# Kernel tuning notes

Hardware: AMD Instinct MI355X
Metric: run time of the kernel (lower is better)

## Reference

```python
import jax, jax.numpy as jnp
import numpy as np

MAX_AREA_WIDTH = 3  # from init_kwargs


def _window_vals(val, width, merge):
    """Multi-scale forward window sums: for each w in 1..width, sum val[t:t+w]
    over the seq axis, concatenated along the seq axis (total length
    width*L - width*(width-1)/2). Equivalent to the torch recurrence."""
    B, H, L, D = val.shape
    csum = jnp.concatenate(
        [jnp.zeros((B, H, 1, D), val.dtype), jnp.cumsum(val, axis=2)], axis=2)
    parts = []
    for i in range(width):
        w = i + 1
        s = csum[:, :, w:, :] - csum[:, :, :L - w + 1, :]  # [B,H,L-i,D]
        if merge == 'mean':
            s = s / jnp.asarray(w, val.dtype)
        parts.append(s)
    return jnp.concatenate(parts, axis=2)


def _window_masks(mask, width, zero_pad):
    parts = [mask[:, :, :, i:] for i in range(width)]
    m = jnp.concatenate(parts, axis=-1)  # [B,H,L,L']
    if zero_pad:
        m = m.at[:, :, 0, :].set(0)
    return m


def setup_inputs() -> dict:
    key = jax.random.key(0)
    kq, kk, kv = jax.random.split(key, 3)
    B, H, L, D = 8, 8, 512, 64
    q = jax.random.normal(kq, (B, H, L, D), jnp.float32)
    k = jax.random.normal(kk, (B, H, L, D), jnp.float32)
    v = jax.random.normal(kv, (B, H, L, D), jnp.float32)
    # causal attention mask, as used in pykt knowledge-tracing models
    mask = jnp.broadcast_to(jnp.tril(jnp.ones((L, L), jnp.int32)), (B, H, L, L))
    return {"q": q, "k": k, "v": v, "d_k": 64, "mask": mask, "zero_pad": 1}


def reference(q, k, v, d_k, mask, zero_pad):
    W = MAX_AREA_WIDTH
    k_area = _window_vals(k, W, 'mean')   # [B,H,L',D]
    v_area = _window_vals(v, W, 'sum')    # [B,H,L',D]
    m = _window_masks(mask, W, zero_pad)  # [B,H,L,L']
    scores = jnp.einsum('bhqd,bhkd->bhqk', q, k_area) / jnp.sqrt(
        jnp.asarray(d_k, jnp.float32))
    scores = jnp.where(m == 0, jnp.asarray(-1e32, scores.dtype), scores)
    attn = jax.nn.softmax(scores, axis=-1)  # dropout omitted (eval / p=0)
    return jnp.einsum('bhqk,bhkd->bhqd', attn, v_area)
```

## Files before the change

kernel.cpp:

```cpp
#include <hip/hip_runtime.h>


#define LSEQ 512
#define DDIM 64
#define SPB 88
#define SSW 68

typedef __attribute__((ext_vector_type(8))) short bf8_t;
typedef __attribute__((ext_vector_type(4))) float f32x4;

__device__ __forceinline__ unsigned short f2bf(float f) {
  union { float f; unsigned u; } v; v.f = f;
  unsigned u = v.u;
  unsigned r = u + 0x7fffu + ((u >> 16) & 1u);
  return (unsigned short)(r >> 16);
}
__device__ __forceinline__ float bf2f(unsigned short h) {
  union { unsigned u; float f; } v; v.u = ((unsigned)h) << 16; return v.f;
}
__device__ __forceinline__ unsigned pk2(float a, float b) {
  return (unsigned)f2bf(a) | ((unsigned)f2bf(b) << 16);
}
__device__ __forceinline__ float ex2(float x) {
  float r; asm("v_exp_f32 %0, %1" : "=v"(r) : "v"(x)); return r;
}

__global__ __launch_bounds__(256)
void prep_kernel(const float* __restrict__ qg, const float* __restrict__ kg,
                 const float* __restrict__ vg,
                 unsigned short* __restrict__ vt,
                 unsigned short* __restrict__ qbf,
                 unsigned short* __restrict__ kbf,
                 float* __restrict__ outg) {
  const int bid = blockIdx.x, tid = threadIdx.x;
  if (bid < 512) {
    const int bh = bid >> 3, oct = bid & 7;
    const float* vb = vg + (size_t)bh * LSEQ * DDIM;
    unsigned short* vo = vt + (size_t)bh * DDIM * LSEQ;
#pragma unroll
    for (int it = 0; it < 4; ++it) {
      int item = tid + it * 256;
      int d = item & 63, tq = item >> 6;
      int t = oct * 64 + tq * 4;
      ushort4 o;
      o.x = f2bf(vb[(t + 0) * DDIM + d]);
      o.y = f2bf(vb[(t + 1) * DDIM + d]);
      o.z = f2bf(vb[(t + 2) * DDIM + d]);
      o.w = f2bf(vb[(t + 3) * DDIM + d]);
      *(ushort4*)&vo[(size_t)d * LSEQ + t] = o;
    }
  } else if (bid < 1536) {
    const bool isq = bid < 1024;
    const float4* src = (const float4*)(isq ? qg : kg);
    ushort4* dst = (ushort4*)(isq ? qbf : kbf);
    const float s = isq ? 0.125f : 1.0f;
    const int blk = bid & 511;
#pragma unroll
    for (int it = 0; it < 4; ++it) {
      int f = blk * 1024 + it * 256 + tid;
      float4 x = src[f];
      ushort4 o;
      o.x = f2bf(x.x * s); o.y = f2bf(x.y * s);
      o.z = f2bf(x.z * s); o.w = f2bf(x.w * s);
      dst[f] = o;
    }
  } else {
    __shared__ float4 red[256];
    const int bh = bid - 1536;
    const float4* vb4 = (const float4*)(vg + (size_t)bh * LSEQ * DDIM);
    const int d4 = tid & 15, rg = tid >> 4;
    float4 acc = make_float4(0.f, 0.f, 0.f, 0.f);
    for (int t = rg; t < LSEQ; t += 16) {
      float c = (t == 0 || t == LSEQ - 1) ? 3.f
              : (t == 1 || t == LSEQ - 2) ? 5.f : 6.f;
      float4 x = vb4[t * 16 + d4];
      acc.x += c * x.x; acc.y += c * x.y; acc.z += c * x.z; acc.w += c * x.w;
    }
    red[rg * 16 + d4] = acc;
    __syncthreads();
    if (rg == 0) {
      float4 sum = make_float4(0.f, 0.f, 0.f, 0.f);
#pragma unroll
      for (int g = 0; g < 16; ++g) {
        float4 x = red[g * 16 + d4];
        sum.x += x.x; sum.y += x.y; sum.z += x.z; sum.w += x.w;
      }
      const float inv = 1.0f / 1533.0f;
      sum.x *= inv; sum.y *= inv; sum.z *= inv; sum.w *= inv;
      ((float4*)(outg + (size_t)bh * LSEQ * DDIM))[d4] = sum;
    }
  }
}

__global__ __launch_bounds__(256, 4)
void area_task_kernel(const unsigned short* __restrict__ qbf,
                      const unsigned short* __restrict__ kbf,
                      const unsigned short* __restrict__ vtg,
                      float* __restrict__ partials) {
  __shared__ __align__(16) float Ss[4][16][SSW];
  __shared__ __align__(16) unsigned short Ps[4][16 * SPB];

  const int w = threadIdx.x >> 6, lane = threadIdx.x & 63;
  const int tau = blockIdx.x * 4 + w;
  const int bh = tau / 144;
  const int idx = tau - bh * 144;
  int g = 0;
  while (2 * (g + 1) * (g + 2) <= idx) ++g;
  const int rem = idx - 2 * g * (g + 1);
  const int dq = rem / (g + 1);
  const int qt = 4 * g + dq;
  const int kt = rem - dq * (g + 1);
  const int q0 = qt * 16, t0 = kt * 64;

  const int lc = lane & 15, lg = lane >> 4;
  const int koff = lg * 8;
  const int pr = lane >> 2, ps = lane & 3;
  const int ec0 = ps * 16;
  const float L2E = 1.44269504088896341f;

  const unsigned short* qb = qbf + (size_t)bh * LSEQ * DDIM;
  const unsigned short* kb = kbf + (size_t)bh * LSEQ * DDIM;
  const unsigned short* vtb = vtg + (size_t)bh * DDIM * LSEQ;

  const bf8_t qa0 = *(const bf8_t*)&qb[(size_t)(q0 + lc) * DDIM + koff];
  const bf8_t qa1 = *(const bf8_t*)&qb[(size_t)(q0 + lc) * DDIM + 32 + koff];

  float val = 0.f;
  if (kt > 0) {
    const int prr = lane >> 2, jj = (lane >> 1) & 1, hh = lane & 1;
    const unsigned short* qrow = qb + (size_t)(q0 + prr) * DDIM + 32 * hh;
    const unsigned short* krow = kb + (size_t)(t0 - 2 + jj) * DDIM + 32 * hh;
#pragma unroll
    for (int b4 = 0; b4 < 4; ++b4) {
      bf8_t qv = *(const bf8_t*)&qrow[b4 * 8];
      bf8_t kv = *(const bf8_t*)&krow[b4 * 8];
#pragma unroll
      for (int e = 0; e < 8; ++e)
        val = fmaf(bf2f((unsigned short)qv[e]), bf2f((unsigned short)kv[e]), val);
    }
    val += __shfl_xor(val, 1);
  }
  const float ctx2 = __shfl(val, lane & ~3);
  const float ctx1 = __shfl(val, (lane & ~3) | 2);

#pragma unroll
  for (int nt = 0; nt < 4; ++nt) {
    const size_t kr = (size_t)(t0 + nt * 16 + lc) * DDIM;
    bf8_t kf0 = *(const bf8_t*)&kb[kr + koff];
    bf8_t kf1 = *(const bf8_t*)&kb[kr + 32 + koff];
    f32x4 acc = (f32x4){0.f, 0.f, 0.f, 0.f};
    acc = __builtin_amdgcn_mfma_f32_16x16x32_bf16(qa0, kf0, acc, 0, 0, 0);
    acc = __builtin_amdgcn_mfma_f32_16x16x32_bf16(qa1, kf1, acc, 0, 0, 0);
#pragma unroll
    for (int r = 0; r < 4; ++r)
      Ss[w][4 * lg + r][nt * 16 + lc] = acc[r];
  }

  float lrow;
  {
    const int vmax = q0 + pr - t0;
    float pm1, pm2;
    if (ps == 0) {
      pm1 = (kt ? ctx1 : -1.0e30f) * L2E;
      pm2 = (kt ? ctx2 : -1.0e30f) * L2E;
    } else {
      pm1 = Ss[w][pr][ec0 - 1] * L2E;
      pm2 = Ss[w][pr][ec0 - 2] * L2E;
    }

    float sv[16];
    *(float4*)&sv[0]  = *(const float4*)&Ss[w][pr][ec0];
    *(float4*)&sv[4]  = *(const float4*)&Ss[w][pr][ec0 + 4];
    *(float4*)&sv[8]  = *(const float4*)&Ss[w][pr][ec0 + 8];
    *(float4*)&sv[12] = *(const float4*)&Ss[w][pr][ec0 + 12];
#pragma unroll
    for (int k = 0; k < 16; ++k) sv[k] *= L2E;

    float cf[18];
#pragma unroll
    for (int k = 0; k < 18; ++k) cf[k] = 0.f;
    float ladd = 0.f;
    {
      float a1 = pm1, a2 = pm2;
#pragma unroll
      for (int k = 0; k < 16; ++k) {
        float s0 = sv[k];
        bool vld = (ec0 + k) <= vmax;
        float t = a1 + s0;
        float p1 = vld ? ex2(s0) : 0.f;
        float p2 = vld ? ex2(0.5f * t) : 0.f;
        float p3 = vld ? ex2((1.0f / 3.0f) * (a2 + t)) : 0.f;
        float p23 = p2 + p3, p123 = p1 + p23;
        ladd += p123;
        cf[k + 2] += p123;
        cf[k + 1] += p23;
        cf[k]     += p3;
        a2 = a1; a1 = s0;
      }
    }
    ladd += __shfl_xor(ladd, 1);
    ladd += __shfl_xor(ladd, 2);
    lrow = ladd;

    float up16 = __shfl_up(cf[16], 1, 4);
    float up17 = __shfl_up(cf[17], 1, 4);
    if (ps > 0) { cf[0] += up16; cf[1] += up17; }

    const int base = pr * SPB;
    if (ps == 0) {
      *(unsigned*)&Ps[w][base + 64] = pk2(cf[0], cf[1]);
#pragma unroll
      for (int j = 0; j < 7; ++j)
        *(unsigned*)&Ps[w][base + 2 * j] = pk2(cf[2 + 2 * j], cf[3 + 2 * j]);
    } else {
      const int tcb = 16 * ps - 2;
#pragma unroll
      for (int j = 0; j < 8; ++j)
        *(unsigned*)&Ps[w][base + tcb + 2 * j] = pk2(cf[2 * j], cf[2 * j + 1]);
      if (ps == 3) *(unsigned*)&Ps[w][base + 62] = pk2(cf[16], cf[17]);
    }
  }

  f32x4 oacc[4];
#pragma unroll
  for (int nt = 0; nt < 4; ++nt) oacc[nt] = (f32x4){0.f, 0.f, 0.f, 0.f};
  {
    bf8_t pa0 = *(const bf8_t*)&Ps[w][lc * SPB + koff];
    bf8_t pa1 = *(const bf8_t*)&Ps[w][lc * SPB + 32 + koff];
    float cm2[4], cm1[4];
#pragma unroll
    for (int r = 0; r < 4; ++r) {
      unsigned pc = *(const unsigned*)&Ps[w][(4 * lg + r) * SPB + 64];
      cm2[r] = bf2f((unsigned short)(pc & 0xffffu));
      cm1[r] = bf2f((unsigned short)(pc >> 16));
    }
#pragma unroll
    for (int nt = 0; nt < 4; ++nt) {
      const size_t vr = (size_t)(nt * 16 + lc) * LSEQ + t0;
      bf8_t vf0 = *(const bf8_t*)&vtb[vr + koff];
      bf8_t vf1 = *(const bf8_t*)&vtb[vr + 32 + koff];
      oacc[nt] = __builtin_amdgcn_mfma_f32_16x16x32_bf16(pa0, vf0, oacc[nt], 0, 0, 0);
      oacc[nt] = __builtin_amdgcn_mfma_f32_16x16x32_bf16(pa1, vf1, oacc[nt], 0, 0, 0);
      unsigned vc = 0;
      if (kt > 0) vc = *(const unsigned*)&vtb[vr - 2];
      float vm2 = bf2f((unsigned short)(vc & 0xffffu));
      float vm1 = bf2f((unsigned short)(vc >> 16));
#pragma unroll
      for (int r = 0; r < 4; ++r)
        oacc[nt][r] += cm2[r] * vm2 + cm1[r] * vm1;
    }
  }

  float* pb = partials + (size_t)tau * 1040;
#pragma unroll
  for (int nt = 0; nt < 4; ++nt)
#pragma unroll
    for (int r = 0; r < 4; ++r)
      pb[(4 * lg + r) * 64 + nt * 16 + lc] = oacc[nt][r];
  if (ps == 0) pb[1024 + pr] = lrow;
}

__global__ __launch_bounds__(256)
void area_reduce_kernel(const float* __restrict__ partials,
                        float* __restrict__ outg) {
  const int w = threadIdx.x >> 6, lane = threadIdx.x & 63;
  const int pair = blockIdx.x * 4 + w;
  const int bh = pair >> 5, qt = pair & 31;
  const int g = qt >> 2, n = g + 1;
  const int start = bh * 144 + 2 * g * (g + 1) + (qt - 4 * g) * (g + 1);
  const int row = lane >> 2, cg = lane & 3;

  f32x4 a0 = {0.f,0.f,0.f,0.f}, a1 = a0, a2 = a0, a3 = a0;
  float la = 0.f;
  for (int t = 0; t < n; ++t) {
    const float* pp = partials + (size_t)(start + t) * 1040;
    const float* pr_ = pp + row * 64 + cg * 16;
    a0 += *(const f32x4*)&pr_[0];
    a1 += *(const f32x4*)&pr_[4];
    a2 += *(const f32x4*)&pr_[8];
    a3 += *(const f32x4*)&pr_[12];
    la += pp[1024 + row];
  }
  const int gr = qt * 16 + row;
  if (gr != 0) {
    const float inv = 1.0f / la;
    float* ob = outg + ((size_t)bh * LSEQ + gr) * DDIM + cg * 16;
    *(f32x4*)&ob[0]  = a0 * inv;
    *(f32x4*)&ob[4]  = a1 * inv;
    *(f32x4*)&ob[8]  = a2 * inv;
    *(f32x4*)&ob[12] = a3 * inv;
  }
}

extern "C" void kernel_launch(void* const* d_in, const int* in_sizes, int n_in,
                              void* d_out, int out_size, void* d_ws, size_t ws_size,
                              hipStream_t stream) {
  (void)in_sizes; (void)n_in; (void)ws_size; (void)out_size;
  const float* q = (const float*)d_in[0];
  const float* k = (const float*)d_in[1];
  const float* v = (const float*)d_in[2];
  float* out = (float*)d_out;

  unsigned short* ws = (unsigned short*)d_ws;
  unsigned short* vt  = ws;
  unsigned short* qbf = ws + 2097152;
  unsigned short* kbf = ws + 2 * 2097152;
  float* partials = (float*)(ws + 3 * 2097152);

  prep_kernel<<<dim3(1600), dim3(256), 0, stream>>>(q, k, v, vt, qbf, kbf, out);
  area_task_kernel<<<dim3(2304), dim3(256), 0, stream>>>(qbf, kbf, vt, partials);
  area_reduce_kernel<<<dim3(512), dim3(256), 0, stream>>>(partials, out);
}
```

Measured before the change: 166.0 us.

## Stage V transpose through LDS and store attention partials as packed bf16

The V transpose in the prep kernel now reads coalesced float4 rows, transposes them through a padded shared-memory tile, and writes 16-element packed bf16 runs per thread instead of doing strided scalar global reads. The split-K attention partials are stored as bf16 in MFMA lane order with a smaller stride, and the reduce kernel reads them in that layout and unpacks them. This cuts global read/write traffic for partials and V prep, at the cost of rounding partial sums to bf16 before reduction, which lowers accuracy. The output writes in the reduce kernel become scalar per-lane stores.

```diff
diff --git a/kernel.cpp b/kernel.cpp
--- a/kernel.cpp
+++ b/kernel.cpp
@@ -5,6 +5,7 @@
 #define DDIM 64
 #define SPB 88
 #define SSW 68
+#define PSTRIDE 528
 
 typedef __attribute__((ext_vector_type(8))) short bf8_t;
 typedef __attribute__((ext_vector_type(4))) float f32x4;
@@ -34,21 +35,30 @@
                  float* __restrict__ outg) {
   const int bid = blockIdx.x, tid = threadIdx.x;
   if (bid < 512) {
+    __shared__ float Ts[64][65];
     const int bh = bid >> 3, oct = bid & 7;
+    const int t0 = oct * 64;
     const float* vb = vg + (size_t)bh * LSEQ * DDIM;
     unsigned short* vo = vt + (size_t)bh * DDIM * LSEQ;
 #pragma unroll
     for (int it = 0; it < 4; ++it) {
-      int item = tid + it * 256;
-      int d = item & 63, tq = item >> 6;
-      int t = oct * 64 + tq * 4;
-      ushort4 o;
-      o.x = f2bf(vb[(t + 0) * DDIM + d]);
-      o.y = f2bf(vb[(t + 1) * DDIM + d]);
-      o.z = f2bf(vb[(t + 2) * DDIM + d]);
-      o.w = f2bf(vb[(t + 3) * DDIM + d]);
-      *(ushort4*)&vo[(size_t)d * LSEQ + t] = o;
-    }
+      int f = tid + it * 256;
+      int t = f >> 4, d4 = f & 15;
+      float4 x = ((const float4*)(vb + (size_t)(t0 + t) * DDIM))[d4];
+      Ts[d4 * 4 + 0][t] = x.x;
+      Ts[d4 * 4 + 1][t] = x.y;
+      Ts[d4 * 4 + 2][t] = x.z;
+      Ts[d4 * 4 + 3][t] = x.w;
+    }
+    __syncthreads();
+    const int d = tid >> 2, tg = tid & 3;
+    unsigned pk[8];
+#pragma unroll
+    for (int j = 0; j < 8; ++j)
+      pk[j] = pk2(Ts[d][tg * 16 + 2 * j], Ts[d][tg * 16 + 2 * j + 1]);
+    uint4* dst = (uint4*)&vo[(size_t)d * LSEQ + t0 + tg * 16];
+    dst[0] = make_uint4(pk[0], pk[1], pk[2], pk[3]);
+    dst[1] = make_uint4(pk[4], pk[5], pk[6], pk[7]);
   } else if (bid < 1536) {
     const bool isq = bid < 1024;
     const float4* src = (const float4*)(isq ? qg : kg);
@@ -251,13 +261,19 @@
     }
   }
 
-  float* pb = partials + (size_t)tau * 1040;
-#pragma unroll
-  for (int nt = 0; nt < 4; ++nt)
-#pragma unroll
-    for (int r = 0; r < 4; ++r)
-      pb[(4 * lg + r) * 64 + nt * 16 + lc] = oacc[nt][r];
-  if (ps == 0) pb[1024 + pr] = lrow;
+  {
+    float* pb = partials + (size_t)tau * PSTRIDE;
+    unsigned pk[8];
+#pragma unroll
+    for (int nt = 0; nt < 4; ++nt) {
+      pk[2 * nt]     = pk2(oacc[nt][0], oacc[nt][1]);
+      pk[2 * nt + 1] = pk2(oacc[nt][2], oacc[nt][3]);
+    }
+    uint4* ob = (uint4*)((unsigned short*)pb + lane * 16);
+    ob[0] = make_uint4(pk[0], pk[1], pk[2], pk[3]);
+    ob[1] = make_uint4(pk[4], pk[5], pk[6], pk[7]);
+    if (ps == 0) pb[512 + pr] = lrow;
+  }
 }
 
 __global__ __launch_bounds__(256)
@@ -268,27 +284,34 @@
   const int bh = pair >> 5, qt = pair & 31;
   const int g = qt >> 2, n = g + 1;
   const int start = bh * 144 + 2 * g * (g + 1) + (qt - 4 * g) * (g + 1);
-  const int row = lane >> 2, cg = lane & 3;
-
-  f32x4 a0 = {0.f,0.f,0.f,0.f}, a1 = a0, a2 = a0, a3 = a0;
-  float la = 0.f;
+  const int lc = lane & 15, lg = lane >> 4;
+
+  float acc[16];
+#pragma unroll
+  for (int e = 0; e < 16; ++e) acc[e] = 0.f;
+  float la[4] = {0.f, 0.f, 0.f, 0.f};
   for (int t = 0; t < n; ++t) {
-    const float* pp = partials + (size_t)(start + t) * 1040;
-    const float* pr_ = pp + row * 64 + cg * 16;
-    a0 += *(const f32x4*)&pr_[0];
-    a1 += *(const f32x4*)&pr_[4];
-    a2 += *(const f32x4*)&pr_[8];
-    a3 += *(const f32x4*)&pr_[12];
-    la += pp[1024 + row];
-  }
-  const int gr = qt * 16 + row;
-  if (gr != 0) {
-    const float inv = 1.0f / la;
-    float* ob = outg + ((size_t)bh * LSEQ + gr) * DDIM + cg * 16;
-    *(f32x4*)&ob[0]  = a0 * inv;
-    *(f32x4*)&ob[4]  = a1 * inv;
-    *(f32x4*)&ob[8]  = a2 * inv;
-    *(f32x4*)&ob[12] = a3 * inv;
+    const float* pp = partials + (size_t)(start + t) * PSTRIDE;
+    const uint4* ob = (const uint4*)((const unsigned short*)pp + lane * 16);
+    uint4 a = ob[0], b = ob[1];
+    const unsigned pkv[8] = {a.x, a.y, a.z, a.w, b.x, b.y, b.z, b.w};
+#pragma unroll
+    for (int j = 0; j < 8; ++j) {
+      acc[2 * j]     += bf2f((unsigned short)(pkv[j] & 0xffffu));
+      acc[2 * j + 1] += bf2f((unsigned short)(pkv[j] >> 16));
+    }
+#pragma unroll
+    for (int r = 0; r < 4; ++r) la[r] += pp[512 + 4 * lg + r];
+  }
+#pragma unroll
+  for (int r = 0; r < 4; ++r) {
+    int gr = qt * 16 + 4 * lg + r;
+    if (gr != 0) {
+      float inv = 1.0f / la[r];
+#pragma unroll
+      for (int nt = 0; nt < 4; ++nt)
+        outg[((size_t)bh * LSEQ + gr) * DDIM + nt * 16 + lc] = acc[nt * 4 + r] * inv;
+    }
   }
 }
 
```

New measurement: 158.3 us. 1.05x faster.
